# Performance work log

Measured on AMD Instinct MI355X. Metric: run time of the kernel, lower is better.

Reference implementation:

```python
import jax, jax.numpy as jnp
import numpy as np

N, L, G, NB = 1024, 30, 10000, 64  # cells, latent, genes, n_batch

def setup_inputs() -> dict:
    key = jax.random.key(0)
    k = jax.random.split(key, 7)
    z = jax.random.normal(k[0], (N, L), dtype=jnp.float32)
    batch_covariate = jax.random.randint(k[1], (N,), 0, NB, dtype=jnp.int32)
    size_factor = jax.random.uniform(k[2], (N, 1), dtype=jnp.float32)
    # learned params
    W_amat = jax.random.normal(k[3], (L, G), dtype=jnp.float32) * 0.05   # Dense(n_out, use_bias=False)
    A_emb = jax.random.normal(k[4], (NB, G, L), dtype=jnp.float32) * 0.05  # Embed(n_batch, n_out*n_in)
    b_emb = jax.random.normal(k[5], (NB, G), dtype=jnp.float32) * 0.05     # Embed(n_batch, n_out)
    px_r = jax.random.normal(k[6], (G,), dtype=jnp.float32)                # param 'px_r'
    return {"z": z, "batch_covariate": batch_covariate, "size_factor": size_factor,
            "W_amat": W_amat, "A_emb": A_emb, "b_emb": b_emb, "px_r": px_r}

def reference(z, batch_covariate, size_factor, W_amat, A_emb, b_emb, px_r):
    # h1 = Dense(n_out, no bias)(z)
    h1 = z @ W_amat                                  # [N, G]
    # dropout is deterministic (training=False) -> identity; stop_gradient as in source
    z_drop = jax.lax.stop_gradient(z)                # [N, L]
    idx = batch_covariate.astype(jnp.int32).reshape(-1)
    A_b = A_emb[idx]                                 # [N, G, L] per-sample gathered matrix
    h2 = jnp.einsum('cgl,cl->cg', A_b, z_drop)       # [N, G]
    h3 = b_emb[idx]                                  # [N, G]
    mu = jax.nn.softplus(h1 + h2 + h3)               # activation = nn.softplus
    mean = mu * size_factor                          # NegativeBinomial mean
    inverse_dispersion = jnp.exp(px_r)               # NegativeBinomial inverse_dispersion
    return mean, inverse_dispersion
```

## Files before the change

### kernel.cpp

```cpp
#include <hip/hip_runtime.h>

#define NCELLS 1024
#define LDIM   30
#define GDIM   10000
#define NBATCH 64
#define GPB    256
#define WGENES 64
#define WCAP   64

typedef unsigned int u32;
typedef unsigned long long u64;

__global__ __launch_bounds__(256, 6) void decoder_kernel(
    const float* __restrict__ z,
    const void*  __restrict__ cand1,
    const void*  __restrict__ cand2,
    const float* __restrict__ W,
    const float* __restrict__ A,
    const float* __restrict__ Bb,
    const float* __restrict__ px,
    float* __restrict__ out)
{
    const int b    = blockIdx.x;
    const int tid  = threadIdx.x;
    const int lane = tid & 63;
    const int wid  = __builtin_amdgcn_readfirstlane(tid >> 6);
    const int g    = blockIdx.y * GPB + wid * WGENES + lane;
    const bool valid = (g < GDIM);
    const int gc   = valid ? g : GDIM - 1;

    __shared__ int wlist[4][WCAP];

    const u32 probe = ((const u32*)cand1)[lane];
    const bool c1_is_int = __all(probe < 64u);
    const int*   bcov = c1_is_int ? (const int*)cand1   : (const int*)cand2;
    const float* sf   = c1_is_int ? (const float*)cand2 : (const float*)cand1;

    float m[LDIM];
    {
        const float2* arow = (const float2*)(A + ((size_t)b * GDIM + gc) * LDIM);
        #pragma unroll
        for (int j = 0; j < LDIM / 2; j++) {
            const float2 av = arow[j];
            m[2 * j]     = W[(size_t)(2 * j)     * GDIM + gc] + av.x;
            m[2 * j + 1] = W[(size_t)(2 * j + 1) * GDIM + gc] + av.y;
        }
    }
    const float h3  = Bb[(size_t)b * GDIM + gc];
    const float pxv = px[gc];

    wlist[wid][lane] = 0;
    int cnt = 0;
    const u64 below = (1ull << lane) - 1ull;
    for (int i0 = 0; i0 < NCELLS; i0 += 64) {
        const int v = bcov[i0 + lane];
        const u64 mb = __ballot(v == b);
        if (v == b) {
            const int pos = cnt + (int)__popcll(mb & below);
            if (pos < WCAP) wlist[wid][pos] = i0 + lane;
        }
        cnt += (int)__popcll(mb);
    }
    const int total = cnt < WCAP ? cnt : WCAP;

    int   myid = wlist[wid][lane];
    float mysf = sf[myid];
    asm volatile("" : "+v"(myid), "+v"(mysf));

    if (valid && b == 0) out[(size_t)NCELLS * GDIM + g] = __expf(pxv);

    int c = 0;
    for (; c + 4 <= total; c += 4) {
        const int cell0 = __builtin_amdgcn_readlane(myid, c);
        const int cell1 = __builtin_amdgcn_readlane(myid, c + 1);
        const int cell2 = __builtin_amdgcn_readlane(myid, c + 2);
        const int cell3 = __builtin_amdgcn_readlane(myid, c + 3);
        const float s0 = __int_as_float(__builtin_amdgcn_readlane(__float_as_int(mysf), c));
        const float s1 = __int_as_float(__builtin_amdgcn_readlane(__float_as_int(mysf), c + 1));
        const float s2 = __int_as_float(__builtin_amdgcn_readlane(__float_as_int(mysf), c + 2));
        const float s3 = __int_as_float(__builtin_amdgcn_readlane(__float_as_int(mysf), c + 3));
        const float* z0 = z + (size_t)cell0 * LDIM;
        const float* z1 = z + (size_t)cell1 * LDIM;
        const float* z2 = z + (size_t)cell2 * LDIM;
        const float* z3 = z + (size_t)cell3 * LDIM;
        float a0 = h3, b0 = 0.f, a1 = h3, b1 = 0.f;
        float a2 = h3, b2 = 0.f, a3 = h3, b3 = 0.f;
        #pragma unroll
        for (int l = 0; l < LDIM; l += 2) {
            a0 = fmaf(m[l],     z0[l],     a0);
            b0 = fmaf(m[l + 1], z0[l + 1], b0);
            a1 = fmaf(m[l],     z1[l],     a1);
            b1 = fmaf(m[l + 1], z1[l + 1], b1);
            a2 = fmaf(m[l],     z2[l],     a2);
            b2 = fmaf(m[l + 1], z2[l + 1], b2);
            a3 = fmaf(m[l],     z3[l],     a3);
            b3 = fmaf(m[l + 1], z3[l + 1], b3);
        }
        float x0 = a0 + b0, x1 = a1 + b1, x2 = a2 + b2, x3 = a3 + b3;
        float p0 = fmaxf(x0, 0.f) + __logf(1.f + __expf(-fabsf(x0)));
        float p1 = fmaxf(x1, 0.f) + __logf(1.f + __expf(-fabsf(x1)));
        float p2 = fmaxf(x2, 0.f) + __logf(1.f + __expf(-fabsf(x2)));
        float p3 = fmaxf(x3, 0.f) + __logf(1.f + __expf(-fabsf(x3)));
        if (valid) {
            __builtin_nontemporal_store(p0 * s0, &out[(size_t)cell0 * GDIM + g]);
            __builtin_nontemporal_store(p1 * s1, &out[(size_t)cell1 * GDIM + g]);
            __builtin_nontemporal_store(p2 * s2, &out[(size_t)cell2 * GDIM + g]);
            __builtin_nontemporal_store(p3 * s3, &out[(size_t)cell3 * GDIM + g]);
        }
    }
    for (; c < total; c++) {
        const int cell0 = __builtin_amdgcn_readlane(myid, c);
        const float s0 = __int_as_float(__builtin_amdgcn_readlane(__float_as_int(mysf), c));
        const float* z0 = z + (size_t)cell0 * LDIM;
        float a0 = h3, b0 = 0.f;
        #pragma unroll
        for (int l = 0; l < LDIM; l += 2) {
            a0 = fmaf(m[l],     z0[l],     a0);
            b0 = fmaf(m[l + 1], z0[l + 1], b0);
        }
        float x0 = a0 + b0;
        float p0 = fmaxf(x0, 0.f) + __logf(1.f + __expf(-fabsf(x0)));
        if (valid)
            __builtin_nontemporal_store(p0 * s0, &out[(size_t)cell0 * GDIM + g]);
    }
}

extern "C" void kernel_launch(void* const* d_in, const int* in_sizes, int n_in,
                              void* d_out, int out_size, void* d_ws, size_t ws_size,
                              hipStream_t stream) {
    const float* z  = nullptr;
    const float* W  = nullptr;
    const float* A  = nullptr;
    const float* Bb = nullptr;
    const float* px = nullptr;
    const void*  p1024[2] = {nullptr, nullptr};
    int n1024 = 0;
    for (int i = 0; i < n_in; i++) {
        switch (in_sizes[i]) {
            case NCELLS * LDIM:        z  = (const float*)d_in[i]; break;
            case LDIM * GDIM:          W  = (const float*)d_in[i]; break;
            case NBATCH * GDIM * LDIM: A  = (const float*)d_in[i]; break;
            case NBATCH * GDIM:        Bb = (const float*)d_in[i]; break;
            case GDIM:                 px = (const float*)d_in[i]; break;
            case NCELLS:
                if (n1024 < 2) p1024[n1024] = d_in[i];
                n1024++;
                break;
            default: break;
        }
    }
    if (!z || !W || !A || !Bb || !px || n1024 != 2) {
        z  = (const float*)d_in[0];
        p1024[0] = d_in[1];
        p1024[1] = d_in[2];
        W  = (const float*)d_in[3];
        A  = (const float*)d_in[4];
        Bb = (const float*)d_in[5];
        px = (const float*)d_in[6];
    }
    float* out = (float*)d_out;

    decoder_kernel<<<dim3(NBATCH, (GDIM + GPB - 1) / GPB), 256, 0, stream>>>(
        z, p1024[0], p1024[1], W, A, Bb, px, out);
}
```

Measured before the change: 175.0 us.

## Stage A tile into LDS via async global_load_lds and vectorize batch scan

Each block's contiguous 256x30 slice of the per-batch A matrix is now loaded cooperatively with direct global-to-LDS async loads, replacing strided per-thread float2 row reads. The batch-index scan uses int4 loads, and it is placed before the W loads so it overlaps with the async copy. Per-thread A values are then read from LDS after a block barrier. The intent is coalesced A traffic and overlap of the A fetch with other setup. In exchange it adds 30KB of shared memory per block, a __syncthreads, and a lower occupancy hint (5 instead of 6).

```diff
diff --git a/kernel.cpp b/kernel.cpp
--- a/kernel.cpp
+++ b/kernel.cpp
@@ -5,13 +5,15 @@
 #define GDIM   10000
 #define NBATCH 64
 #define GPB    256
-#define WGENES 64
 #define WCAP   64
 
 typedef unsigned int u32;
 typedef unsigned long long u64;
 
-__global__ __launch_bounds__(256, 6) void decoder_kernel(
+#define GLOBAL_AS __attribute__((address_space(1)))
+#define LDS_AS    __attribute__((address_space(3)))
+
+__global__ __launch_bounds__(256, 5) void decoder_kernel(
     const float* __restrict__ z,
     const void*  __restrict__ cand1,
     const void*  __restrict__ cand2,
@@ -25,47 +27,78 @@
     const int tid  = threadIdx.x;
     const int lane = tid & 63;
     const int wid  = __builtin_amdgcn_readfirstlane(tid >> 6);
-    const int g    = blockIdx.y * GPB + wid * WGENES + lane;
+    const int g    = blockIdx.y * GPB + tid;
     const bool valid = (g < GDIM);
     const int gc   = valid ? g : GDIM - 1;
 
+    __shared__ __align__(16) float a_sh[GPB * LDIM];
     __shared__ int wlist[4][WCAP];
+
+    const size_t abase = ((size_t)b * GDIM + (size_t)blockIdx.y * GPB) * LDIM;
+    const size_t atot  = (size_t)NBATCH * GDIM * LDIM;
+    #pragma unroll
+    for (int k = 0; k < 7; k++) {
+        size_t gidx = abase + (size_t)(k * 256 + tid) * 4;
+        if (gidx + 4 > atot) gidx = atot - 4;
+        __builtin_amdgcn_global_load_lds(
+            (const GLOBAL_AS void*)(A + gidx),
+            (LDS_AS void*)(a_sh + k * 1024 + wid * 256), 16, 0, 0);
+    }
+    if (tid < 128) {
+        size_t gidx = abase + (size_t)(1792 + tid) * 4;
+        if (gidx + 4 > atot) gidx = atot - 4;
+        __builtin_amdgcn_global_load_lds(
+            (const GLOBAL_AS void*)(A + gidx),
+            (LDS_AS void*)(a_sh + 7168 + wid * 256), 16, 0, 0);
+    }
 
     const u32 probe = ((const u32*)cand1)[lane];
     const bool c1_is_int = __all(probe < 64u);
     const int*   bcov = c1_is_int ? (const int*)cand1   : (const int*)cand2;
     const float* sf   = c1_is_int ? (const float*)cand2 : (const float*)cand1;
 
-    float m[LDIM];
-    {
-        const float2* arow = (const float2*)(A + ((size_t)b * GDIM + gc) * LDIM);
+    wlist[wid][lane] = 0;
+    int cnt = 0;
+    const u64 below = (1ull << lane) - 1ull;
+    const int4* b4 = (const int4*)bcov;
+    #pragma unroll
+    for (int i0 = 0; i0 < 4; i0++) {
+        const int4 v = b4[i0 * 64 + lane];
+        const int base = i0 * 256 + lane * 4;
         #pragma unroll
-        for (int j = 0; j < LDIM / 2; j++) {
-            const float2 av = arow[j];
-            m[2 * j]     = W[(size_t)(2 * j)     * GDIM + gc] + av.x;
-            m[2 * j + 1] = W[(size_t)(2 * j + 1) * GDIM + gc] + av.y;
+        for (int j = 0; j < 4; j++) {
+            const int vj = (j == 0) ? v.x : (j == 1) ? v.y : (j == 2) ? v.z : v.w;
+            const u64 mb = __ballot(vj == b);
+            if (vj == b) {
+                const int pos = cnt + (int)__popcll(mb & below);
+                if (pos < WCAP) wlist[wid][pos] = base + j;
+            }
+            cnt += (int)__popcll(mb);
         }
     }
+    const int total = cnt < WCAP ? cnt : WCAP;
+
+    float m[LDIM];
+    #pragma unroll
+    for (int l = 0; l < LDIM; l++) m[l] = W[(size_t)l * GDIM + gc];
     const float h3  = Bb[(size_t)b * GDIM + gc];
     const float pxv = px[gc];
 
-    wlist[wid][lane] = 0;
-    int cnt = 0;
-    const u64 below = (1ull << lane) - 1ull;
-    for (int i0 = 0; i0 < NCELLS; i0 += 64) {
-        const int v = bcov[i0 + lane];
-        const u64 mb = __ballot(v == b);
-        if (v == b) {
-            const int pos = cnt + (int)__popcll(mb & below);
-            if (pos < WCAP) wlist[wid][pos] = i0 + lane;
-        }
-        cnt += (int)__popcll(mb);
-    }
-    const int total = cnt < WCAP ? cnt : WCAP;
+    __syncthreads();
 
     int   myid = wlist[wid][lane];
     float mysf = sf[myid];
     asm volatile("" : "+v"(myid), "+v"(mysf));
+
+    {
+        const float2* ar = (const float2*)(a_sh + tid * LDIM);
+        #pragma unroll
+        for (int j = 0; j < LDIM / 2; j++) {
+            const float2 w2 = ar[j];
+            m[2 * j]     += w2.x;
+            m[2 * j + 1] += w2.y;
+        }
+    }
 
     if (valid && b == 0) out[(size_t)NCELLS * GDIM + g] = __expf(pxv);
 
```

New measurement: 161.1 us. 7.9% less time.
